# Performance work log

Measured on AMD Instinct MI355X. Metric: run time of the kernel, lower is better.

Reference implementation:

```python
import jax, jax.numpy as jnp
import numpy as np

NQ = 18          # num_qubits
DEPTH = 3        # circuit_depth
DIM = 2 ** NQ    # state-vector length
STATE_DIM = 256
HIDDEN = 64
ACTION_DIM = 18
BATCH = 4096


def _apply_1q(sv, g, q):
    # apply 2x2 gate g to qubit q (qubit 0 = most-significant index bit, matching the kron order)
    pre, post = 2 ** q, 2 ** (NQ - q - 1)
    s = sv.reshape(pre, 2, post)
    return jnp.einsum('ab,ibj->iaj', g, s).reshape(-1)


def _apply_cnot(sv, at):
    # CNOT with target at reshape-axis `at`, control at axis `at+1` (adjacent, control less significant)
    pre, post = 2 ** at, 2 ** (NQ - at - 2)
    s = sv.reshape(pre, 2, 2, post)           # (pre, target, control, post)
    out = jnp.stack([s[:, :, 0, :], s[:, ::-1, 1, :]], axis=2)
    return out.reshape(-1)


def _circuit(theta, xc):
    sv = jnp.zeros(DIM, jnp.complex64).at[0].set(1.0)
    th = theta.reshape(DEPTH, NQ, 3)
    for layer in range(DEPTH):
        for q in range(NQ):
            a, b, c = th[layer, q, 0], th[layer, q, 1], th[layer, q, 2]
            ca = jnp.cos(a / 2).astype(jnp.complex64)
            sa = jnp.sin(a / 2).astype(jnp.complex64)
            rx = jnp.stack([jnp.stack([ca, -1j * sa]), jnp.stack([-1j * sa, ca])])
            cb = jnp.cos(b / 2).astype(jnp.complex64)
            sb = jnp.sin(b / 2).astype(jnp.complex64)
            ry = jnp.stack([jnp.stack([cb, -sb]), jnp.stack([sb, cb])])
            ez = jnp.exp(-0.5j * c.astype(jnp.complex64))
            z0 = jnp.zeros_like(ez)
            rz = jnp.stack([jnp.stack([ez, z0]), jnp.stack([z0, jnp.conj(ez)])])
            sv = _apply_1q(sv, rx, q)
            sv = _apply_1q(sv, ry, q)
            sv = _apply_1q(sv, rz, q)
        # original CNOT uses little-endian bit positions: control=q -> axis NQ-1-q, target=q+1 -> axis NQ-2-q
        for q in range(NQ - 1):
            sv = _apply_cnot(sv, NQ - 2 - q)
    # _encode_classical_input: flatten, normalize, add into state prefix, renormalize
    x = xc.reshape(-1)
    xn = jnp.linalg.norm(x)
    x = jnp.where(xn > 0, x / xn.astype(jnp.complex64), x)
    m = min(DIM, x.shape[0])
    sv = sv.at[:m].add(x[:m])
    return sv / jnp.linalg.norm(sv).astype(jnp.complex64)


def setup_inputs() -> dict:
    key = jax.random.key(0)
    ks = jax.random.split(key, 16)
    r = lambda k, shp, s: jax.random.normal(k, shp, jnp.float32) * s
    return {
        'state': r(ks[0], (BATCH, STATE_DIM), 1.0),
        'enc_w1': r(ks[1], (STATE_DIM, HIDDEN), 0.06),
        'enc_b1': jnp.zeros((HIDDEN,), jnp.float32),
        'enc_w2': r(ks[2], (HIDDEN, 2 * NQ), 0.12),
        'enc_b2': jnp.zeros((2 * NQ,), jnp.float32),
        'qparams': r(ks[3], (DEPTH * NQ * 3,), 0.1),
        'dec_w1': r(ks[4], (2 * DIM, HIDDEN), 0.0015),
        'dec_b1': jnp.zeros((HIDDEN,), jnp.float32),
        'dec_w2': r(ks[5], (HIDDEN, ACTION_DIM), 0.12),
        'dec_b2': jnp.zeros((ACTION_DIM,), jnp.float32),
        'val_w1': r(ks[6], (2 * DIM, HIDDEN), 0.0015),
        'val_b1': jnp.zeros((HIDDEN,), jnp.float32),
        'val_w2': r(ks[7], (HIDDEN, 1), 0.12),
        'val_b2': jnp.zeros((1,), jnp.float32),
    }


def reference(state, enc_w1, enc_b1, enc_w2, enc_b2, qparams,
              dec_w1, dec_b1, dec_w2, dec_b2,
              val_w1, val_b1, val_w2, val_b2):
    h = jax.nn.relu(state @ enc_w1 + enc_b1)
    enc = h @ enc_w2 + enc_b2                     # [B, 2*NQ]
    amp, ph = enc[:, :NQ], enc[:, NQ:]
    xc = amp.astype(jnp.complex64) * jnp.exp(1j * ph.astype(jnp.complex64))  # torch.polar
    sv = _circuit(qparams, xc)                    # [2^NQ] complex64
    cl = jnp.concatenate([sv.real, sv.imag])      # [2^(NQ+1)] float32
    logits = jax.nn.relu(cl @ dec_w1 + dec_b1) @ dec_w2 + dec_b2
    value = jax.nn.relu(cl @ val_w1 + val_b1) @ val_w2 + val_b2
    return logits, value
```

## Files before the change

kernel.cpp:

```cpp
#include <hip/hip_runtime.h>
#include <cstdint>
#include <cstddef>


#define NQb   18
#define DIMSZ 262144
#define PMASK 0x3FFFF
#define XLEN  73728

typedef float2 cplx;

__device__ __forceinline__ cplx cmul(cplx a, cplx b) {
  return make_float2(a.x*b.x - a.y*b.y, a.x*b.y + a.y*b.x);
}
__device__ __forceinline__ cplx cadd(cplx a, cplx b) {
  return make_float2(a.x + b.x, a.y + b.y);
}

__global__ void k_prep(const float* __restrict__ qp, cplx* __restrict__ Ug,
                       cplx* __restrict__ prodLow, cplx* __restrict__ prodHigh,
                       float* __restrict__ accs) {
  __shared__ cplx Ush[54][4];
  int t = threadIdx.x;
  if (t < 132) accs[t] = 0.0f;
  if (t < 54) {
    float a = qp[t*3+0], b = qp[t*3+1], c = qp[t*3+2];
    float ca = cosf(0.5f*a), sa = sinf(0.5f*a);
    float cb = cosf(0.5f*b), sb = sinf(0.5f*b);
    float cc = cosf(0.5f*c), sc = sinf(0.5f*c);
    cplx m00 = make_float2( cb*ca,  sb*sa);
    cplx m01 = make_float2(-sb*ca, -cb*sa);
    cplx m10 = make_float2( sb*ca, -cb*sa);
    cplx m11 = make_float2( cb*ca, -sb*sa);
    cplx e0 = make_float2(cc, -sc), e1 = make_float2(cc, sc);
    cplx u00 = cmul(e0, m00), u01 = cmul(e0, m01);
    cplx u10 = cmul(e1, m10), u11 = cmul(e1, m11);
    Ush[t][0] = u00; Ush[t][1] = u01; Ush[t][2] = u10; Ush[t][3] = u11;
    Ug[t*4+0] = u00; Ug[t*4+1] = u01; Ug[t*4+2] = u10; Ug[t*4+3] = u11;
  }
  __syncthreads();
  for (int m = t; m < 4096; m += blockDim.x) {
    cplx v = make_float2(1.f, 0.f);
    for (int p = 0; p < 12; ++p) {
      int q = 17 - p;
      cplx f = ((m >> p) & 1) ? Ush[q][2] : Ush[q][0];
      v = cmul(v, f);
    }
    prodLow[m] = v;
  }
  if (t < 64) {
    cplx v = make_float2(1.f, 0.f);
    for (int p = 12; p < 18; ++p) {
      int q = 17 - p;
      cplx f = ((t >> (p - 12)) & 1) ? Ush[q][2] : Ush[q][0];
      v = cmul(v, f);
    }
    prodHigh[t] = v;
  }
}

__global__ __launch_bounds__(256) void k_enc(
    const float* __restrict__ state, const float* __restrict__ w1,
    const float* __restrict__ b1, const float* __restrict__ w2,
    const float* __restrict__ b2, float* __restrict__ xRe,
    float* __restrict__ xIm, float* __restrict__ xn2) {
  __shared__ float sState[4][256];
  __shared__ float hS[4][64];
  __shared__ float encS[4][36];
  __shared__ float wsum[4];
  int t = threadIdx.x;
  int r = t >> 6, j = t & 63;
  const float4* st4 =
      reinterpret_cast<const float4*>(state + (size_t)blockIdx.x * 1024);
  reinterpret_cast<float4*>(&sState[0][0])[t] = st4[t];
  __syncthreads();
  float a0 = 0.f, a1 = 0.f, a2 = 0.f, a3 = 0.f;
#pragma unroll 4
  for (int k = 0; k < 256; k += 4) {
    a0 = fmaf(sState[r][k+0], w1[(k+0)*64 + j], a0);
    a1 = fmaf(sState[r][k+1], w1[(k+1)*64 + j], a1);
    a2 = fmaf(sState[r][k+2], w1[(k+2)*64 + j], a2);
    a3 = fmaf(sState[r][k+3], w1[(k+3)*64 + j], a3);
  }
  hS[r][j] = fmaxf((a0 + a1) + (a2 + a3) + b1[j], 0.f);
  __syncthreads();
  if (j < 36) {
    float a = b2[j];
#pragma unroll 8
    for (int k = 0; k < 64; ++k) a = fmaf(hS[r][k], w2[k*36 + j], a);
    encS[r][j] = a;
  }
  __syncthreads();
  float lsum = 0.f;
  if (j < 18) {
    float amp = encS[r][j], ph = encS[r][18 + j];
    float sp, cp;
    sincosf(ph, &sp, &cp);
    int row = blockIdx.x*4 + r;
    xRe[row*18 + j] = amp * cp;
    xIm[row*18 + j] = amp * sp;
    lsum = amp * amp;
  }
  for (int off = 32; off > 0; off >>= 1) lsum += __shfl_down(lsum, off, 64);
  if (j == 0) wsum[r] = lsum;
  __syncthreads();
  if (t == 0) atomicAdd(xn2, wsum[0] + wsum[1] + wsum[2] + wsum[3]);
}

__global__ __launch_bounds__(512) void k_sweepA(
    const cplx* __restrict__ Ug, const cplx* __restrict__ prodLow,
    const cplx* __restrict__ prodHigh, const cplx* __restrict__ svIn,
    cplx* __restrict__ svOut, int layer, int mode) {
  __shared__ float sRe[4096], sIm[4096];
  int t = threadIdx.x;
  int base = blockIdx.x << 12;
  for (int e = t; e < 4096; e += 512) {
    int i = base + e;
    int src = (i ^ (i << 1)) & PMASK;
    cplx v;
    if (mode == 0) v = cmul(prodHigh[src >> 12], prodLow[src & 4095]);
    else           v = svIn[src];
    sRe[e] = v.x; sIm[e] = v.y;
  }
  __syncthreads();
  for (int p = 0; p < 12; ++p) {
    int q = 17 - p;
    const cplx* U = Ug + (layer*18 + q)*4;
    cplx u00 = U[0], u01 = U[1], u10 = U[2], u11 = U[3];
    for (int k = t; k < 2048; k += 512) {
      int i0 = ((k >> p) << (p + 1)) | (k & ((1 << p) - 1));
      int i1 = i0 | (1 << p);
      cplx a = make_float2(sRe[i0], sIm[i0]);
      cplx b = make_float2(sRe[i1], sIm[i1]);
      cplx na = cadd(cmul(u00, a), cmul(u01, b));
      cplx nb = cadd(cmul(u10, a), cmul(u11, b));
      sRe[i0] = na.x; sIm[i0] = na.y;
      sRe[i1] = nb.x; sIm[i1] = nb.y;
    }
    __syncthreads();
  }
  for (int e = t; e < 4096; e += 512)
    svOut[base + e] = make_float2(sRe[e], sIm[e]);
}

__global__ __launch_bounds__(512) void k_sweepB(const cplx* __restrict__ Ug,
                                                cplx* __restrict__ sv,
                                                int layer) {
  __shared__ float tRe[4096], tIm[4096];
  int t = threadIdx.x;
  int lbase = blockIdx.x << 6;
  for (int m = t; m < 4096; m += 512) {
    int h = m >> 6, l = m & 63;
    cplx v = sv[h*4096 + lbase + l];
    tRe[m] = v.x; tIm[m] = v.y;
  }
  __syncthreads();
  for (int ph = 0; ph < 6; ++ph) {
    int p = 12 + ph, q = 17 - p;
    const cplx* U = Ug + (layer*18 + q)*4;
    cplx u00 = U[0], u01 = U[1], u10 = U[2], u11 = U[3];
    for (int k = t; k < 2048; k += 512) {
      int kh = k >> 6, l = k & 63;
      int h0 = ((kh >> ph) << (ph + 1)) | (kh & ((1 << ph) - 1));
      int h1 = h0 | (1 << ph);
      int i0 = h0*64 + l, i1 = h1*64 + l;
      cplx a = make_float2(tRe[i0], tIm[i0]);
      cplx b = make_float2(tRe[i1], tIm[i1]);
      cplx na = cadd(cmul(u00, a), cmul(u01, b));
      cplx nb = cadd(cmul(u10, a), cmul(u11, b));
      tRe[i0] = na.x; tIm[i0] = na.y;
      tRe[i1] = nb.x; tIm[i1] = nb.y;
    }
    __syncthreads();
  }
  for (int m = t; m < 4096; m += 512) {
    int h = m >> 6, l = m & 63;
    sv[h*4096 + lbase + l] = make_float2(tRe[m], tIm[m]);
  }
}

__global__ __launch_bounds__(256) void k_combine(
    const cplx* __restrict__ svIn, const float* __restrict__ xRe,
    const float* __restrict__ xIm, const float* __restrict__ xn2,
    float* __restrict__ cl, float* __restrict__ L2acc) {
  int t = threadIdx.x;
  float xs = xn2[0];
  float invXn = (xs > 0.f) ? (1.0f / sqrtf(xs)) : 1.0f;
  float lsum = 0.f;
  for (int u = 0; u < 4; ++u) {
    int i = blockIdx.x*1024 + u*256 + t;
    int src = (i ^ (i << 1)) & PMASK;
    cplx v = svIn[src];
    if (i < XLEN) {
      v.x = fmaf(xRe[i], invXn, v.x);
      v.y = fmaf(xIm[i], invXn, v.y);
    }
    cl[i] = v.x;
    cl[DIMSZ + i] = v.y;
    lsum += v.x*v.x + v.y*v.y;
  }
  for (int off = 32; off > 0; off >>= 1) lsum += __shfl_down(lsum, off, 64);
  if ((t & 63) == 0) atomicAdd(L2acc, lsum);
}

__global__ __launch_bounds__(256) void k_matvec(
    const float* __restrict__ cl, const float* __restrict__ Wdec,
    const float* __restrict__ Wval, const float* __restrict__ L2acc,
    float* __restrict__ dots) {
  __shared__ float clS[1024];
  __shared__ float red[1024];
  int t = threadIdx.x;
  int mat = blockIdx.x & 1;
  size_t r0 = (size_t)(blockIdx.x >> 1) * 1024;
  const float4* cl4 = reinterpret_cast<const float4*>(cl + r0);
  reinterpret_cast<float4*>(clS)[t] = cl4[t];
  __syncthreads();
  const float* W = (mat ? Wval : Wdec) + r0*64 + (size_t)((t & 15)*4);
  int ro = t >> 4;
  float ax = 0.f, ay = 0.f, az = 0.f, aw = 0.f;
#pragma unroll 4
  for (int pass = 0; pass < 64; ++pass) {
    int r = (pass << 4) + ro;
    const float4 w = *reinterpret_cast<const float4*>(W + (size_t)r*64);
    float s = clS[r];
    ax = fmaf(s, w.x, ax);
    ay = fmaf(s, w.y, ay);
    az = fmaf(s, w.z, az);
    aw = fmaf(s, w.w, aw);
  }
  red[t*4+0] = ax; red[t*4+1] = ay; red[t*4+2] = az; red[t*4+3] = aw;
  __syncthreads();
  if (t < 64) {
    int ci0 = t >> 2, jj = t & 3;
    float sum = 0.f;
    for (int r2 = 0; r2 < 16; ++r2) sum += red[(r2*16 + ci0)*4 + jj];
    float invL = 1.0f / sqrtf(L2acc[0]);
    atomicAdd(&dots[mat*64 + t], sum * invL);
  }
}

__global__ void k_final(const float* __restrict__ dots,
                        const float* __restrict__ db1,
                        const float* __restrict__ dw2,
                        const float* __restrict__ db2,
                        const float* __restrict__ vb1,
                        const float* __restrict__ vw2,
                        const float* __restrict__ vb2,
                        float* __restrict__ out) {
  __shared__ float hd[64], hv[64];
  int t = threadIdx.x;
  hd[t] = fmaxf(dots[t] + db1[t], 0.f);
  hv[t] = fmaxf(dots[64 + t] + vb1[t], 0.f);
  __syncthreads();
  if (t < 18) {
    float s = db2[t];
    for (int k = 0; k < 64; ++k) s = fmaf(hd[k], dw2[k*18 + t], s);
    out[t] = s;
  }
  if (t == 20) {
    float s = vb2[0];
    for (int k = 0; k < 64; ++k) s = fmaf(hv[k], vw2[k], s);
    out[18] = s;
  }
}

extern "C" void kernel_launch(void* const* d_in, const int* in_sizes, int n_in,
                              void* d_out, int out_size, void* d_ws,
                              size_t ws_size, hipStream_t stream) {
  const float* state  = (const float*)d_in[0];
  const float* enc_w1 = (const float*)d_in[1];
  const float* enc_b1 = (const float*)d_in[2];
  const float* enc_w2 = (const float*)d_in[3];
  const float* enc_b2 = (const float*)d_in[4];
  const float* qparams= (const float*)d_in[5];
  const float* dec_w1 = (const float*)d_in[6];
  const float* dec_b1 = (const float*)d_in[7];
  const float* dec_w2 = (const float*)d_in[8];
  const float* dec_b2 = (const float*)d_in[9];
  const float* val_w1 = (const float*)d_in[10];
  const float* val_b1 = (const float*)d_in[11];
  const float* val_w2 = (const float*)d_in[12];
  const float* val_b2 = (const float*)d_in[13];

  float* wsf = (float*)d_ws;
  float* dots     = wsf;
  float* xn2      = wsf + 128;
  float* L2acc    = wsf + 129;
  cplx*  Ug       = (cplx*)(wsf + 256);
  cplx*  prodLow  = (cplx*)(wsf + 1024);
  cplx*  prodHigh = (cplx*)(wsf + 9216);
  float* xRe      = wsf + 16384;
  float* xIm      = wsf + 90112;
  cplx*  svA      = (cplx*)(wsf + 163840);
  cplx*  svB      = (cplx*)(wsf + 688128);
  float* cl       = wsf + 1212416;

  hipLaunchKernelGGL(k_prep, dim3(1), dim3(256), 0, stream,
                     qparams, Ug, prodLow, prodHigh, wsf);
  hipLaunchKernelGGL(k_enc, dim3(1024), dim3(256), 0, stream,
                     state, enc_w1, enc_b1, enc_w2, enc_b2, xRe, xIm, xn2);
  hipLaunchKernelGGL(k_sweepA, dim3(64), dim3(512), 0, stream,
                     Ug, prodLow, prodHigh, (const cplx*)nullptr, svA, 1, 0);
  hipLaunchKernelGGL(k_sweepB, dim3(64), dim3(512), 0, stream, Ug, svA, 1);
  hipLaunchKernelGGL(k_sweepA, dim3(64), dim3(512), 0, stream,
                     Ug, prodLow, prodHigh, (const cplx*)svA, svB, 2, 1);
  hipLaunchKernelGGL(k_sweepB, dim3(64), dim3(512), 0, stream, Ug, svB, 2);
  hipLaunchKernelGGL(k_combine, dim3(256), dim3(256), 0, stream,
                     svB, xRe, xIm, xn2, cl, L2acc);
  hipLaunchKernelGGL(k_matvec, dim3(1024), dim3(256), 0, stream,
                     cl, dec_w1, val_w1, L2acc, dots);
  hipLaunchKernelGGL(k_final, dim3(1), dim3(64), 0, stream,
                     dots, dec_b1, dec_w2, dec_b2, val_b1, val_w2, val_b2,
                     (float*)d_out);
}
```

Measured before the change: 401.2 us.

## Split gate sweeps into smaller tiles and spread matvec atomics across slots

The state-vector gate passes are re-tiled from 4096-element tiles to 1024-element tiles. The low pass now handles 10 qubits and the high pass 8, so each launch uses 256 blocks instead of 64 and occupies more CUs. The matvec now uses 512-row chunks and batches 8 weight loads before the FMAs to raise memory-level parallelism. Its atomics go to 32 replicated accumulator slots, which k_final sums and then scales by the 1/L2 norm, to cut atomic contention. The trade-off is more global round-trips per element in the gate passes, since each tile covers fewer qubits, plus a larger zeroed workspace.

```diff
diff --git a/kernel.cpp b/kernel.cpp
--- a/kernel.cpp
+++ b/kernel.cpp
@@ -22,7 +22,7 @@
                        float* __restrict__ accs) {
   __shared__ cplx Ush[54][4];
   int t = threadIdx.x;
-  if (t < 132) accs[t] = 0.0f;
+  for (int k = t; k < 4352; k += 256) accs[k] = 0.0f;
   if (t < 54) {
     float a = qp[t*3+0], b = qp[t*3+1], c = qp[t*3+2];
     float ca = cosf(0.5f*a), sa = sinf(0.5f*a);
@@ -107,14 +107,14 @@
   if (t == 0) atomicAdd(xn2, wsum[0] + wsum[1] + wsum[2] + wsum[3]);
 }
 
-__global__ __launch_bounds__(512) void k_sweepA(
+__global__ __launch_bounds__(512) void k_gatesLow(
     const cplx* __restrict__ Ug, const cplx* __restrict__ prodLow,
     const cplx* __restrict__ prodHigh, const cplx* __restrict__ svIn,
     cplx* __restrict__ svOut, int layer, int mode) {
-  __shared__ float sRe[4096], sIm[4096];
-  int t = threadIdx.x;
-  int base = blockIdx.x << 12;
-  for (int e = t; e < 4096; e += 512) {
+  __shared__ float sRe[1024], sIm[1024];
+  int t = threadIdx.x;
+  int base = blockIdx.x << 10;
+  for (int e = t; e < 1024; e += 512) {
     int i = base + e;
     int src = (i ^ (i << 1)) & PMASK;
     cplx v;
@@ -123,11 +123,12 @@
     sRe[e] = v.x; sIm[e] = v.y;
   }
   __syncthreads();
-  for (int p = 0; p < 12; ++p) {
+  for (int p = 0; p < 10; ++p) {
     int q = 17 - p;
     const cplx* U = Ug + (layer*18 + q)*4;
     cplx u00 = U[0], u01 = U[1], u10 = U[2], u11 = U[3];
-    for (int k = t; k < 2048; k += 512) {
+    if (t < 512) {
+      int k = t;
       int i0 = ((k >> p) << (p + 1)) | (k & ((1 << p) - 1));
       int i1 = i0 | (1 << p);
       cplx a = make_float2(sRe[i0], sIm[i0]);
@@ -139,31 +140,30 @@
     }
     __syncthreads();
   }
-  for (int e = t; e < 4096; e += 512)
+  for (int e = t; e < 1024; e += 512)
     svOut[base + e] = make_float2(sRe[e], sIm[e]);
 }
 
-__global__ __launch_bounds__(512) void k_sweepB(const cplx* __restrict__ Ug,
-                                                cplx* __restrict__ sv,
-                                                int layer) {
-  __shared__ float tRe[4096], tIm[4096];
-  int t = threadIdx.x;
-  int lbase = blockIdx.x << 6;
-  for (int m = t; m < 4096; m += 512) {
-    int h = m >> 6, l = m & 63;
-    cplx v = sv[h*4096 + lbase + l];
-    tRe[m] = v.x; tIm[m] = v.y;
-  }
-  __syncthreads();
-  for (int ph = 0; ph < 6; ++ph) {
-    int p = 12 + ph, q = 17 - p;
+__global__ __launch_bounds__(512) void k_gatesHigh(
+    const cplx* __restrict__ Ug, cplx* __restrict__ sv, int layer) {
+  __shared__ float tRe[1024], tIm[1024];
+  int t = threadIdx.x;
+  int l0 = blockIdx.x << 2;
+  for (int e = t; e < 1024; e += 512) {
+    int h = e >> 2, j = e & 3;
+    cplx v = sv[h*1024 + l0 + j];
+    tRe[e] = v.x; tIm[e] = v.y;
+  }
+  __syncthreads();
+  for (int ph = 0; ph < 8; ++ph) {
+    int q = 7 - ph;
     const cplx* U = Ug + (layer*18 + q)*4;
     cplx u00 = U[0], u01 = U[1], u10 = U[2], u11 = U[3];
-    for (int k = t; k < 2048; k += 512) {
-      int kh = k >> 6, l = k & 63;
+    if (t < 512) {
+      int kh = t >> 2, j = t & 3;
       int h0 = ((kh >> ph) << (ph + 1)) | (kh & ((1 << ph) - 1));
       int h1 = h0 | (1 << ph);
-      int i0 = h0*64 + l, i1 = h1*64 + l;
+      int i0 = h0*4 + j, i1 = h1*4 + j;
       cplx a = make_float2(tRe[i0], tIm[i0]);
       cplx b = make_float2(tRe[i1], tIm[i1]);
       cplx na = cadd(cmul(u00, a), cmul(u01, b));
@@ -173,9 +173,9 @@
     }
     __syncthreads();
   }
-  for (int m = t; m < 4096; m += 512) {
-    int h = m >> 6, l = m & 63;
-    sv[h*4096 + lbase + l] = make_float2(tRe[m], tIm[m]);
+  for (int e = t; e < 1024; e += 512) {
+    int h = e >> 2, j = e & 3;
+    sv[h*1024 + l0 + j] = make_float2(tRe[e], tIm[e]);
   }
 }
 
@@ -203,43 +203,53 @@
   if ((t & 63) == 0) atomicAdd(L2acc, lsum);
 }
 
-__global__ __launch_bounds__(256) void k_matvec(
+__global__ __launch_bounds__(256, 4) void k_matvec(
     const float* __restrict__ cl, const float* __restrict__ Wdec,
-    const float* __restrict__ Wval, const float* __restrict__ L2acc,
-    float* __restrict__ dots) {
-  __shared__ float clS[1024];
+    const float* __restrict__ Wval, float* __restrict__ dots_rep) {
+  __shared__ float clS[512];
   __shared__ float red[1024];
   int t = threadIdx.x;
   int mat = blockIdx.x & 1;
-  size_t r0 = (size_t)(blockIdx.x >> 1) * 1024;
-  const float4* cl4 = reinterpret_cast<const float4*>(cl + r0);
-  reinterpret_cast<float4*>(clS)[t] = cl4[t];
+  int chunk = blockIdx.x >> 1;
+  size_t r0 = (size_t)chunk * 512;
+  if (t < 128)
+    reinterpret_cast<float4*>(clS)[t] =
+        reinterpret_cast<const float4*>(cl + r0)[t];
   __syncthreads();
   const float* W = (mat ? Wval : Wdec) + r0*64 + (size_t)((t & 15)*4);
   int ro = t >> 4;
   float ax = 0.f, ay = 0.f, az = 0.f, aw = 0.f;
-#pragma unroll 4
-  for (int pass = 0; pass < 64; ++pass) {
-    int r = (pass << 4) + ro;
-    const float4 w = *reinterpret_cast<const float4*>(W + (size_t)r*64);
-    float s = clS[r];
-    ax = fmaf(s, w.x, ax);
-    ay = fmaf(s, w.y, ay);
-    az = fmaf(s, w.z, az);
-    aw = fmaf(s, w.w, aw);
+  for (int g = 0; g < 4; ++g) {
+    float4 w[8];
+    float  s[8];
+#pragma unroll
+    for (int u = 0; u < 8; ++u) {
+      int r = g*128 + u*16 + ro;
+      w[u] = *reinterpret_cast<const float4*>(W + (size_t)r*64);
+      s[u] = clS[r];
+    }
+#pragma unroll
+    for (int u = 0; u < 8; ++u) {
+      ax = fmaf(s[u], w[u].x, ax);
+      ay = fmaf(s[u], w[u].y, ay);
+      az = fmaf(s[u], w[u].z, az);
+      aw = fmaf(s[u], w[u].w, aw);
+    }
   }
   red[t*4+0] = ax; red[t*4+1] = ay; red[t*4+2] = az; red[t*4+3] = aw;
   __syncthreads();
   if (t < 64) {
     int ci0 = t >> 2, jj = t & 3;
     float sum = 0.f;
+#pragma unroll
     for (int r2 = 0; r2 < 16; ++r2) sum += red[(r2*16 + ci0)*4 + jj];
-    float invL = 1.0f / sqrtf(L2acc[0]);
-    atomicAdd(&dots[mat*64 + t], sum * invL);
-  }
-}
-
-__global__ void k_final(const float* __restrict__ dots,
+    int slot = chunk & 31;
+    atomicAdd(&dots_rep[slot*128 + mat*64 + t], sum);
+  }
+}
+
+__global__ void k_final(const float* __restrict__ dots_rep,
+                        const float* __restrict__ L2acc,
                         const float* __restrict__ db1,
                         const float* __restrict__ dw2,
                         const float* __restrict__ db2,
@@ -249,8 +259,15 @@
                         float* __restrict__ out) {
   __shared__ float hd[64], hv[64];
   int t = threadIdx.x;
-  hd[t] = fmaxf(dots[t] + db1[t], 0.f);
-  hv[t] = fmaxf(dots[64 + t] + vb1[t], 0.f);
+  float sd = 0.f, sva = 0.f;
+#pragma unroll
+  for (int s = 0; s < 32; ++s) {
+    sd  += dots_rep[s*128 + t];
+    sva += dots_rep[s*128 + 64 + t];
+  }
+  float invL = 1.0f / sqrtf(L2acc[0]);
+  hd[t] = fmaxf(sd * invL + db1[t], 0.f);
+  hv[t] = fmaxf(sva * invL + vb1[t], 0.f);
   __syncthreads();
   if (t < 18) {
     float s = db2[t];
@@ -283,33 +300,33 @@
   const float* val_b2 = (const float*)d_in[13];
 
   float* wsf = (float*)d_ws;
-  float* dots     = wsf;
-  float* xn2      = wsf + 128;
-  float* L2acc    = wsf + 129;
-  cplx*  Ug       = (cplx*)(wsf + 256);
-  cplx*  prodLow  = (cplx*)(wsf + 1024);
-  cplx*  prodHigh = (cplx*)(wsf + 9216);
-  float* xRe      = wsf + 16384;
-  float* xIm      = wsf + 90112;
-  cplx*  svA      = (cplx*)(wsf + 163840);
-  cplx*  svB      = (cplx*)(wsf + 688128);
-  float* cl       = wsf + 1212416;
+  float* dots_rep = wsf;
+  float* xn2      = wsf + 4096;
+  float* L2acc    = wsf + 4097;
+  cplx*  Ug       = (cplx*)(wsf + 4352);
+  cplx*  prodLow  = (cplx*)(wsf + 8192);
+  cplx*  prodHigh = (cplx*)(wsf + 16384);
+  float* xRe      = wsf + 16640;
+  float* xIm      = wsf + 90368;
+  cplx*  svA      = (cplx*)(wsf + 164096);
+  cplx*  svB      = (cplx*)(wsf + 688384);
+  float* cl       = wsf + 1212672;
 
   hipLaunchKernelGGL(k_prep, dim3(1), dim3(256), 0, stream,
                      qparams, Ug, prodLow, prodHigh, wsf);
   hipLaunchKernelGGL(k_enc, dim3(1024), dim3(256), 0, stream,
                      state, enc_w1, enc_b1, enc_w2, enc_b2, xRe, xIm, xn2);
-  hipLaunchKernelGGL(k_sweepA, dim3(64), dim3(512), 0, stream,
+  hipLaunchKernelGGL(k_gatesLow, dim3(256), dim3(512), 0, stream,
                      Ug, prodLow, prodHigh, (const cplx*)nullptr, svA, 1, 0);
-  hipLaunchKernelGGL(k_sweepB, dim3(64), dim3(512), 0, stream, Ug, svA, 1);
-  hipLaunchKernelGGL(k_sweepA, dim3(64), dim3(512), 0, stream,
+  hipLaunchKernelGGL(k_gatesHigh, dim3(256), dim3(512), 0, stream, Ug, svA, 1);
+  hipLaunchKernelGGL(k_gatesLow, dim3(256), dim3(512), 0, stream,
                      Ug, prodLow, prodHigh, (const cplx*)svA, svB, 2, 1);
-  hipLaunchKernelGGL(k_sweepB, dim3(64), dim3(512), 0, stream, Ug, svB, 2);
+  hipLaunchKernelGGL(k_gatesHigh, dim3(256), dim3(512), 0, stream, Ug, svB, 2);
   hipLaunchKernelGGL(k_combine, dim3(256), dim3(256), 0, stream,
                      svB, xRe, xIm, xn2, cl, L2acc);
-  hipLaunchKernelGGL(k_matvec, dim3(1024), dim3(256), 0, stream,
-                     cl, dec_w1, val_w1, L2acc, dots);
+  hipLaunchKernelGGL(k_matvec, dim3(2048), dim3(256), 0, stream,
+                     cl, dec_w1, val_w1, dots_rep);
   hipLaunchKernelGGL(k_final, dim3(1), dim3(64), 0, stream,
-                     dots, dec_b1, dec_w2, dec_b2, val_b1, val_w2, val_b2,
-                     (float*)d_out);
-}
+                     dots_rep, L2acc, dec_b1, dec_w2, dec_b2,
+                     val_b1, val_w2, val_b2, (float*)d_out);
+}
```

Result: faster. 387.5 us (-3.4%).
